# Kernel optimization log

Measured on AMD Instinct MI355X. Metric: run time of the kernel, lower is better.

The kernel has to match this reference:

```python
import math
import jax, jax.numpy as jnp
import numpy as np

D = 512
H = 8
N_COLS = 2048            # n + 1
D_COL = math.ceil(2 * math.log2(N_COLS))  # 22
B = 8
N_KEEP = 768
T = N_KEEP + 1


def setup_inputs() -> dict:
    key = jax.random.key(0)
    ks = jax.random.split(key, 12)
    inp = {
        "x_head": jax.random.normal(ks[0], (B, T, D), jnp.float32),
        "x_tail": jax.random.normal(ks[1], (B, T, D), jnp.float32),
        "ids_keep": jax.random.randint(ks[2], (B, N_KEEP), 0, N_COLS - 1),
        # W_tail is tied to W_head (sym_weight=True)
        "W_head_w": jax.random.normal(ks[3], (D, D), jnp.float32) * (1.0 / math.sqrt(D)),
        "W_head_b": jnp.zeros((D,), jnp.float32),
        "W_v_w": jax.random.normal(ks[4], (D, D), jnp.float32) * (1.0 / math.sqrt(D)),
        "W_v_b": jnp.zeros((D,), jnp.float32),
        "W_out_w": jax.random.normal(ks[5], (D, D), jnp.float32) * (1.0 / math.sqrt(D)),
        "W_out_b": jnp.zeros((D,), jnp.float32),
        "rel_emb": jnp.ones((H, D // H), jnp.float32),
        "col_head": jax.random.normal(ks[6], (H, N_COLS, D_COL), jnp.float32),
        "col_tail": jax.random.normal(ks[7], (H, N_COLS, D_COL), jnp.float32),
        "bias": jnp.zeros((1,), jnp.float32),
    }
    return inp


def _split_heads(x, n_heads):
    b, t, d = x.shape
    return x.reshape(b, t, n_heads, d // n_heads).transpose(0, 2, 1, 3)  # [B,H,T,dh]


def _gather_cols(col_emb, ids_keep):
    """col_emb: [H, N_COLS, d_col] (L2-normalized). Gather kept feature rows per
    batch element and re-prepend the CLS/readout row -> [B, H, 1+n_keep, d_col]."""
    cls = col_emb[:, :1, :]                       # [H,1,dc]
    feats = col_emb[:, 1:, :]                     # [H,N_COLS-1,dc]
    kept = jnp.take(feats, ids_keep, axis=1)      # [H,B,nk,dc]
    kept = kept.transpose(1, 0, 2, 3)             # [B,H,nk,dc]
    cls_b = jnp.broadcast_to(cls[None], (kept.shape[0],) + cls.shape)  # [B,H,1,dc]
    return jnp.concatenate([cls_b, kept], axis=2)


def reference(x_head, x_tail, ids_keep, W_head_w, W_head_b, W_v_w, W_v_b,
              W_out_w, W_out_b, rel_emb, col_head, col_tail, bias):
    n_heads = rel_emb.shape[0]
    d_head = rel_emb.shape[1]
    b, t, _ = x_head.shape

    # Projections (W_tail tied to W_head)
    f_head = x_head @ W_head_w.T + W_head_b
    f_tail = x_tail @ W_head_w.T + W_head_b
    f_v = x_tail @ W_v_w.T + W_v_b

    fh = _split_heads(f_head, n_heads)  # [B,H,T,dh]
    ft = _split_heads(f_tail, n_heads)
    fv = _split_heads(f_v, n_heads)

    # relation-weighted score: f_head @ diag(rel_emb) @ f_tail^T / sqrt(dh)
    weight_score = jnp.einsum('bhqd,bhkd->bhqk', fh * rel_emb[None, :, None, :], ft)
    weight_score = weight_score / math.sqrt(d_head)

    # Normalized topology embeddings + masked-token gather
    ch = col_head / jnp.linalg.norm(col_head, axis=-1, keepdims=True)
    ct = col_tail / jnp.linalg.norm(col_tail, axis=-1, keepdims=True)
    ch = _gather_cols(ch, ids_keep)  # [B,H,T,dc]
    ct = _gather_cols(ct, ids_keep)
    top_score = jnp.einsum('bhqd,bhkd->bhqk', ch, ct)  # [B,H,T,T]

    # Topology -> straight-through binary adjacency
    adj_probs = jax.nn.sigmoid(top_score + bias[0])
    nsi_mask = 1.0 - jnp.eye(t, dtype=adj_probs.dtype)          # no self-interaction
    adj_probs = adj_probs * nsi_mask
    readout_mask = jnp.ones((t,), adj_probs.dtype).at[0].set(0.0)  # prune edges to readout
    adj_probs = adj_probs * readout_mask
    adj = (adj_probs > 0.5).astype(adj_probs.dtype) - jax.lax.stop_gradient(adj_probs) + adj_probs

    adj_mask = (1.0 - adj) * -10000.0
    fr_graph = jax.nn.softmax(weight_score + adj_mask, axis=-1)

    x = jnp.einsum('bhqk,bhkd->bhqd', fr_graph, fv)
    x = x.transpose(0, 2, 1, 3).reshape(b, t, n_heads * fv.shape[-1])
    x = x @ W_out_w.T + W_out_b
    return (x, jax.lax.stop_gradient(fr_graph))
```

## Files before the change

### kernel.cpp

```cpp
#include <hip/hip_runtime.h>

#define D_     512
#define H_     8
#define NCOLS_ 2048
#define DCOL_  22
#define B_     8
#define NKEEP_ 768
#define T_     769
#define BT_    (B_*T_)
#define BH_    (B_*H_)

typedef __attribute__((ext_vector_type(8))) short bf16x8;
typedef __attribute__((ext_vector_type(8))) _Float16 f16x8;
typedef __attribute__((ext_vector_type(4))) float f32x4;

__device__ __forceinline__ ushort f2bf(float f) {
    unsigned u = __float_as_uint(f);
    unsigned r = u + 0x7fffu + ((u >> 16) & 1u);
    return (ushort)(r >> 16);
}
__device__ __forceinline__ float bf2f(ushort u) {
    return __uint_as_float(((unsigned)u) << 16);
}

__device__ __attribute__((noinline)) float exact_dot22(
    const float* __restrict__ qp, const float* __restrict__ kp)
{
    float s = 0.f;
    #pragma unroll
    for (int d2 = 0; d2 < DCOL_; ++d2) s += qp[d2]*kp[d2];
    return s;
}

__global__ __launch_bounds__(256) void pre_all(
    const float* __restrict__ xh, const float* __restrict__ xt,
    const float* __restrict__ Wh, const float* __restrict__ Wv,
    const float* __restrict__ bh_, const float* __restrict__ bv_,
    const float* __restrict__ rel,
    ushort* __restrict__ fhb, ushort* __restrict__ ftb,
    ushort* __restrict__ fvb,
    const float* __restrict__ col_head, const float* __restrict__ col_tail,
    const int* __restrict__ ids,
    float* __restrict__ chg, float* __restrict__ ctg,
    ushort* __restrict__ chH, ushort* __restrict__ chL,
    ushort* __restrict__ ctH, ushort* __restrict__ ctL)
{
    __shared__ __align__(16) ushort As[128*40];
    __shared__ __align__(16) ushort Bs[128*40];
    const int job = blockIdx.z;
    const int t   = threadIdx.x;

    if (job == 3) {
        const int total = BH_ * T_;
        const int stride = 4*49*256;
        for (int r = ((int)blockIdx.y*4 + (int)blockIdx.x)*256 + t;
             r < 2*total; r += stride) {
            const bool tail = (r >= total);
            int rr = tail ? r - total : r;
            int bh = rr / T_;
            int q  = rr - bh*T_;
            int b  = bh >> 3, h = bh & 7;
            int src = (q == 0) ? 0 : (1 + ids[b*NKEEP_ + q - 1]);
            const float* cp = (tail ? col_tail : col_head) + ((size_t)h*NCOLS_ + src)*DCOL_;
            float v[DCOL_];
            float ss = 0.f;
            #pragma unroll
            for (int j = 0; j < DCOL_; ++j) { v[j] = cp[j]; ss += v[j]*v[j]; }
            float inv = 1.0f / sqrtf(ss);
            float* op = (tail ? ctg : chg) + (size_t)rr*DCOL_;
            ushort* hp = (tail ? ctH : chH) + (size_t)rr*32;
            ushort* lp = (tail ? ctL : chL) + (size_t)rr*32;
            #pragma unroll
            for (int j = 0; j < DCOL_; ++j) {
                float x = v[j]*inv;
                op[j] = x;
                float xs = x * 32.f;
                _Float16 hh = (_Float16)xs;
                float res = (xs - (float)hh) * 2048.f;
                _Float16 ll = (_Float16)res;
                hp[j] = __builtin_bit_cast(ushort, hh);
                lp[j] = __builtin_bit_cast(ushort, ll);
            }
            #pragma unroll
            for (int j = DCOL_; j < 32; ++j) { hp[j] = 0; lp[j] = 0; }
        }
        return;
    }

    const float* A32; const float* W; const float* bias;
    ushort* outb; int mode;
    if (job == 0)      { A32 = xh; W = Wh; bias = bh_; outb = fhb; mode = 0; }
    else if (job == 1) { A32 = xt; W = Wh; bias = bh_; outb = ftb; mode = 1; }
    else               { A32 = xt; W = Wv; bias = bv_; outb = fvb; mode = 2; }

    const int lane = t & 63;
    const int wv   = t >> 6;
    const int wr   = wv >> 1, wc = wv & 1;
    const int m16  = lane & 15, q4 = lane >> 4;
    const int m0   = blockIdx.y * 128;
    const int n0   = blockIdx.x * 128;

    f32x4 acc[4][4] = {};
    for (int k0 = 0; k0 < 512; k0 += 32) {
        {
            const int sr = t >> 1, sh = t & 1;
            const int row = m0 + sr;
            ushort ta[16];
            #pragma unroll
            for (int e = 0; e < 16; ++e) ta[e] = 0;
            if (row < BT_) {
                const float* ap = A32 + (size_t)row*512 + k0 + sh*16;
                #pragma unroll
                for (int e = 0; e < 4; ++e) {
                    float4 f = *(const float4*)(ap + e*4);
                    ta[e*4+0]=f2bf(f.x); ta[e*4+1]=f2bf(f.y);
                    ta[e*4+2]=f2bf(f.z); ta[e*4+3]=f2bf(f.w);
                }
            }
            *(bf16x8*)&As[sr*40 + sh*16]     = *(bf16x8*)&ta[0];
            *(bf16x8*)&As[sr*40 + sh*16 + 8] = *(bf16x8*)&ta[8];
            const float* wp = W + (size_t)(n0 + sr)*512 + k0 + sh*16;
            ushort tw[16];
            #pragma unroll
            for (int e = 0; e < 4; ++e) {
                float4 f = *(const float4*)(wp + e*4);
                tw[e*4+0]=f2bf(f.x); tw[e*4+1]=f2bf(f.y);
                tw[e*4+2]=f2bf(f.z); tw[e*4+3]=f2bf(f.w);
            }
            *(bf16x8*)&Bs[sr*40 + sh*16]     = *(bf16x8*)&tw[0];
            *(bf16x8*)&Bs[sr*40 + sh*16 + 8] = *(bf16x8*)&tw[8];
        }
        __syncthreads();
        bf16x8 a[4], b[4];
        #pragma unroll
        for (int i = 0; i < 4; ++i)
            a[i] = *(const bf16x8*)&As[(wr*64 + i*16 + m16)*40 + q4*8];
        #pragma unroll
        for (int j = 0; j < 4; ++j)
            b[j] = *(const bf16x8*)&Bs[(wc*64 + j*16 + m16)*40 + q4*8];
        #pragma unroll
        for (int i = 0; i < 4; ++i)
            #pragma unroll
            for (int j = 0; j < 4; ++j)
                acc[i][j] = __builtin_amdgcn_mfma_f32_16x16x32_bf16(a[i], b[j], acc[i][j], 0, 0, 0);
        __syncthreads();
    }

    #pragma unroll
    for (int j = 0; j < 4; ++j) {
        const int n = n0 + wc*64 + j*16 + m16;
        const float bn = bias[n];
        const float sc = (mode == 0) ? rel[n] * 0.125f : 1.0f;
        const int h = n >> 6, dh = n & 63;
        #pragma unroll
        for (int i = 0; i < 4; ++i) {
            #pragma unroll
            for (int r = 0; r < 4; ++r) {
                int m = m0 + wr*64 + i*16 + q4*4 + r;
                if (m >= BT_) continue;
                float v = acc[i][j][r] + bn;
                if (mode == 0) v *= sc;
                int bb = m / T_, tt = m - bb*T_;
                outb[(((size_t)bb*H_ + h)*T_ + tt)*64 + dh] = f2bf(v);
            }
        }
    }
}

__global__ __launch_bounds__(256, 3) void fused_attn(
    const ushort* __restrict__ fhb, const ushort* __restrict__ ftb,
    const ushort* __restrict__ fvb, const float* __restrict__ chg,
    const float* __restrict__ ctg,
    const ushort* __restrict__ chH, const ushort* __restrict__ chL,
    const ushort* __restrict__ ctH, const ushort* __restrict__ ctL,
    const float* __restrict__ biasp,
    float* __restrict__ fr, ushort* __restrict__ x1b, float* __restrict__ invA)
{
    __shared__ __align__(16) ushort Qs[64*72];
    __shared__ __align__(16) ushort Ks[64*72];
    __shared__ __align__(16) ushort Vs[64*72];
    __shared__ __align__(16) ushort Et[64*72];
    __shared__ __align__(16) ushort KH[64*40];
    __shared__ __align__(16) ushort KL[64*40];
    __shared__ float sumP[4*64];
    __shared__ float inv_s[64];

    const int bh = blockIdx.y;
    const int q0 = blockIdx.x * 64;

    const int t    = threadIdx.x;
    const int lane = t & 63, w = t >> 6;
    const int m16  = lane & 15, q4 = lane >> 4;
    const float bias0 = biasp[0];

    {
        int qr = t >> 2, qc = min(q0 + qr, T_-1);
        const ushort* qp = fhb + ((size_t)bh*T_ + qc)*64 + (t&3)*16;
        *(bf16x8*)&Qs[qr*72 + (t&3)*16]     = *(const bf16x8*)qp;
        *(bf16x8*)&Qs[qr*72 + (t&3)*16 + 8] = *(const bf16x8*)(qp + 8);
    }
    f16x8 gqh[4], gql[4];
    #pragma unroll
    for (int i = 0; i < 4; ++i) {
        int qc = min(q0 + i*16 + m16, T_-1);
        gqh[i] = *(const f16x8*)(chH + ((size_t)bh*T_ + qc)*32 + q4*8);
        gql[i] = *(const f16x8*)(chL + ((size_t)bh*T_ + qc)*32 + q4*8);
    }

    float psum[4][4] = {};
    f32x4 Oacc[4] = {};

    for (int kt = 0; kt < 13; ++kt) {
        const int k0g = kt*64;
        __syncthreads();

        {
            int kr = t >> 2, kc = min(k0g + kr, T_-1);
            const ushort* kp = ftb + ((size_t)bh*T_ + kc)*64 + (t&3)*16;
            *(bf16x8*)&Ks[kr*72 + (t&3)*16]     = *(const bf16x8*)kp;
            *(bf16x8*)&Ks[kr*72 + (t&3)*16 + 8] = *(const bf16x8*)(kp + 8);
            const ushort* vp = fvb + ((size_t)bh*T_ + kc)*64 + (t&3)*16;
            bf16x8 v0 = *(const bf16x8*)vp, v1 = *(const bf16x8*)(vp + 8);
            const int dbase = (t&3)*16;
            #pragma unroll
            for (int e = 0; e < 8; ++e) {
                int d = dbase + e;
                Vs[d*72 + (((kr>>3) ^ (d>>3))<<3) + (kr&7)] = (ushort)v0[e];
            }
            #pragma unroll
            for (int e = 0; e < 8; ++e) {
                int d = dbase + 8 + e;
                Vs[d*72 + (((kr>>3) ^ (d>>3))<<3) + (kr&7)] = (ushort)v1[e];
            }
            const ushort* hp = ctH + ((size_t)bh*T_ + kc)*32 + (t&3)*8;
            const ushort* lp = ctL + ((size_t)bh*T_ + kc)*32 + (t&3)*8;
            *(bf16x8*)&KH[kr*40 + (t&3)*8] = *(const bf16x8*)hp;
            *(bf16x8*)&KL[kr*40 + (t&3)*8] = *(const bf16x8*)lp;
        }
        __syncthreads();

        const int kL2 = w*16 + m16;
        const int kg  = k0g + kL2;
        unsigned kmask = 0;
        {
            f16x8 bhf = *(const f16x8*)&KH[kL2*40 + q4*8];
            f16x8 blf = *(const f16x8*)&KL[kL2*40 + q4*8];
            f32x4 G1[4] = {}; f32x4 G2[4] = {};
            #pragma unroll
            for (int i = 0; i < 4; ++i) {
                G1[i] = __builtin_amdgcn_mfma_f32_16x16x32_f16(gqh[i], bhf, G1[i], 0, 0, 0);
                G2[i] = __builtin_amdgcn_mfma_f32_16x16x32_f16(gqh[i], blf, G2[i], 0, 0, 0);
                G2[i] = __builtin_amdgcn_mfma_f32_16x16x32_f16(gql[i], bhf, G2[i], 0, 0, 0);
            }
            const bool kok = (kg != 0) && (kg < T_);
            if (kok) {
                const float bS = bias0 * 1024.f;
                #pragma unroll
                for (int i = 0; i < 4; ++i) {
                    #pragma unroll
                    for (int r = 0; r < 4; ++r) {
                        int qg = q0 + i*16 + q4*4 + r;
                        if (qg == kg) continue;
                        float sd = G1[i][r] + G2[i][r]*(1.0f/2048.0f) + bS;
                        bool keep = sd > 0.f;
                        if (__builtin_fabsf(sd) <= 0.16f && qg < T_) {
                            float s = exact_dot22(chg + ((size_t)bh*T_ + qg)*DCOL_,
                                                  ctg + ((size_t)bh*T_ + kg)*DCOL_);
                            keep = (s + bias0 > 0.f);
                        }
                        if (keep) kmask |= 1u << (i*4 + r);
                    }
                }
            }
        }

        f32x4 Sacc[4] = {};
        #pragma unroll
        for (int step = 0; step < 2; ++step) {
            bf16x8 b = *(const bf16x8*)&Ks[kL2*72 + step*32 + q4*8];
            #pragma unroll
            for (int i = 0; i < 4; ++i) {
                bf16x8 a = *(const bf16x8*)&Qs[(i*16 + m16)*72 + step*32 + q4*8];
                Sacc[i] = __builtin_amdgcn_mfma_f32_16x16x32_bf16(a, b, Sacc[i], 0, 0, 0);
            }
        }

        #pragma unroll
        for (int i = 0; i < 4; ++i) {
            #pragma unroll
            for (int r = 0; r < 4; ++r) {
                float e = ((kmask >> (i*4 + r)) & 1u) ? __expf(Sacc[i][r]) : 0.f;
                psum[i][r] += e;
                Et[(i*16 + q4*4 + r)*72 + kL2] = f2bf(e);
            }
        }
        __syncthreads();

        #pragma unroll
        for (int step = 0; step < 2; ++step) {
            bf16x8 a = *(const bf16x8*)&Et[(w*16 + m16)*72 + step*32 + q4*8];
            #pragma unroll
            for (int j = 0; j < 4; ++j) {
                int dv = j*16 + m16;
                bf16x8 b = *(const bf16x8*)&Vs[dv*72 + (((step*4 + q4) ^ (dv>>3))<<3)];
                Oacc[j] = __builtin_amdgcn_mfma_f32_16x16x32_bf16(a, b, Oacc[j], 0, 0, 0);
            }
        }

        {
            const int c = t & 15;
            #pragma unroll
            for (int p = 0; p < 4; ++p) {
                int row = p*16 + (t >> 4);
                int qg = q0 + row;
                if (qg >= T_) continue;
                char* rowbase = (char*)(fr + ((size_t)bh*T_ + qg)*T_);
                #pragma unroll
                for (int e = 0; e < 2; ++e) {
                    int dw = c + 16*e;
                    int kk = k0g + dw*2;
                    unsigned u = *(const unsigned*)&Et[row*72 + dw*2];
                    if (kk + 1 < T_)
                        __builtin_nontemporal_store(u, (unsigned*)(rowbase + (size_t)kk*2));
                    else if (kk < T_)
                        __builtin_nontemporal_store((ushort)u, (ushort*)(rowbase + (size_t)kk*2));
                }
            }
        }
    }

    #pragma unroll
    for (int i = 0; i < 4; ++i)
        #pragma unroll
        for (int r = 0; r < 4; ++r) {
            float v = psum[i][r];
            v += __shfl_xor(v, 1, 64);
            v += __shfl_xor(v, 2, 64);
            v += __shfl_xor(v, 4, 64);
            v += __shfl_xor(v, 8, 64);
            psum[i][r] = v;
        }
    if (m16 == 0) {
        #pragma unroll
        for (int i = 0; i < 4; ++i)
            #pragma unroll
            for (int r = 0; r < 4; ++r)
                sumP[w*64 + i*16 + q4*4 + r] = psum[i][r];
    }
    __syncthreads();
    if (t < 64) {
        float s = sumP[t] + sumP[64+t] + sumP[128+t] + sumP[192+t];
        float iv = 1.0f / fmaxf(s, 1e-30f);
        inv_s[t] = iv;
        if (q0 + t < T_) invA[(size_t)bh*T_ + q0 + t] = iv;
    }
    __syncthreads();

    {
        const int b = bh >> 3, h = bh & 7;
        #pragma unroll
        for (int j = 0; j < 4; ++j) {
            int d = j*16 + m16;
            #pragma unroll
            for (int r = 0; r < 4; ++r) {
                int rr = w*16 + q4*4 + r;
                int qg = q0 + rr;
                if (qg < T_)
                    x1b[((size_t)b*T_ + qg)*512 + h*64 + d] = f2bf(Oacc[j][r] * inv_s[rr]);
            }
        }
    }
}

__global__ __launch_bounds__(256) void post_all(
    const ushort* __restrict__ x1b, const float* __restrict__ Wo,
    const float* __restrict__ bo_,
    float* __restrict__ xout, float* __restrict__ fr,
    const float* __restrict__ invA)
{
    __shared__ __align__(16) ushort As[128*40];
    __shared__ __align__(16) ushort Bs[128*40];
    const int bid = blockIdx.x;
    const int t   = threadIdx.x;

    if (bid >= 196) {
        const int row = bid - 196;
        float* rowp = fr + (size_t)row * T_;
        const ushort* packed = (const ushort*)rowp;
        const float iv = invA[row];
        float v0 = bf2f(packed[t])       * iv;
        float v1 = bf2f(packed[t + 256]) * iv;
        float v2 = bf2f(packed[t + 512]) * iv;
        float v3 = 0.f;
        if (t == 0) v3 = bf2f(packed[768]) * iv;
        __syncthreads();
        __builtin_nontemporal_store(v0, rowp + t);
        __builtin_nontemporal_store(v1, rowp + t + 256);
        __builtin_nontemporal_store(v2, rowp + t + 512);
        if (t == 0) __builtin_nontemporal_store(v3, rowp + 768);
        return;
    }

    const int lane = t & 63;
    const int wv   = t >> 6;
    const int wr   = wv >> 1, wc = wv & 1;
    const int m16  = lane & 15, q4 = lane >> 4;
    const int n0   = (bid & 3) * 128;
    const int m0   = (bid >> 2) * 128;

    f32x4 acc[4][4] = {};
    for (int k0 = 0; k0 < 512; k0 += 32) {
        {
            const int sr = t >> 1, sh = t & 1;
            const int row = m0 + sr;
            bf16x8 z = {}; bf16x8 v0 = z, v1 = z;
            if (row < BT_) {
                const bf16x8* gp = (const bf16x8*)(x1b + (size_t)row*512 + k0 + sh*16);
                v0 = gp[0]; v1 = gp[1];
            }
            *(bf16x8*)&As[sr*40 + sh*16]     = v0;
            *(bf16x8*)&As[sr*40 + sh*16 + 8] = v1;
            const float* wp = Wo + (size_t)(n0 + sr)*512 + k0 + sh*16;
            ushort tw[16];
            #pragma unroll
            for (int e = 0; e < 4; ++e) {
                float4 f = *(const float4*)(wp + e*4);
                tw[e*4+0]=f2bf(f.x); tw[e*4+1]=f2bf(f.y);
                tw[e*4+2]=f2bf(f.z); tw[e*4+3]=f2bf(f.w);
            }
            *(bf16x8*)&Bs[sr*40 + sh*16]     = *(bf16x8*)&tw[0];
            *(bf16x8*)&Bs[sr*40 + sh*16 + 8] = *(bf16x8*)&tw[8];
        }
        __syncthreads();
        bf16x8 a[4], b[4];
        #pragma unroll
        for (int i = 0; i < 4; ++i)
            a[i] = *(const bf16x8*)&As[(wr*64 + i*16 + m16)*40 + q4*8];
        #pragma unroll
        for (int j = 0; j < 4; ++j)
            b[j] = *(const bf16x8*)&Bs[(wc*64 + j*16 + m16)*40 + q4*8];
        #pragma unroll
        for (int i = 0; i < 4; ++i)
            #pragma unroll
            for (int j = 0; j < 4; ++j)
                acc[i][j] = __builtin_amdgcn_mfma_f32_16x16x32_bf16(a[i], b[j], acc[i][j], 0, 0, 0);
        __syncthreads();
    }

    #pragma unroll
    for (int j = 0; j < 4; ++j) {
        const int n = n0 + wc*64 + j*16 + m16;
        const float bn = bo_[n];
        #pragma unroll
        for (int i = 0; i < 4; ++i) {
            #pragma unroll
            for (int r = 0; r < 4; ++r) {
                int m = m0 + wr*64 + i*16 + q4*4 + r;
                if (m >= BT_) continue;
                __builtin_nontemporal_store(acc[i][j][r] + bn, xout + (size_t)m*512 + n);
            }
        }
    }
}

extern "C" void kernel_launch(void* const* d_in, const int* in_sizes, int n_in,
                              void* d_out, int out_size, void* d_ws, size_t ws_size,
                              hipStream_t stream)
{
    (void)in_sizes; (void)n_in; (void)out_size; (void)ws_size;
    const float* x_head   = (const float*)d_in[0];
    const float* x_tail   = (const float*)d_in[1];
    const int*   ids      = (const int*)  d_in[2];
    const float* W_head_w = (const float*)d_in[3];
    const float* W_head_b = (const float*)d_in[4];
    const float* W_v_w    = (const float*)d_in[5];
    const float* W_v_b    = (const float*)d_in[6];
    const float* W_out_w  = (const float*)d_in[7];
    const float* W_out_b  = (const float*)d_in[8];
    const float* rel      = (const float*)d_in[9];
    const float* col_h    = (const float*)d_in[10];
    const float* col_t    = (const float*)d_in[11];
    const float* biasp    = (const float*)d_in[12];

    const size_t F   = (size_t)BH_*T_*64;
    const size_t C22 = (size_t)BH_*T_*DCOL_;
    const size_t C32 = (size_t)BH_*T_*32;

    char* ws = (char*)d_ws;
    ushort* fhb = (ushort*)ws;   ws += F*2;
    ushort* ftb = (ushort*)ws;   ws += F*2;
    ushort* fvb = (ushort*)ws;   ws += F*2;
    ushort* x1b = (ushort*)ws;   ws += F*2;
    float*  chg = (float*)ws;    ws += C22*4;
    float*  ctg = (float*)ws;    ws += C22*4;
    float*  invA = (float*)ws;   ws += (size_t)BH_*T_*4;
    ushort* chH = (ushort*)ws;   ws += C32*2;
    ushort* chL = (ushort*)ws;   ws += C32*2;
    ushort* ctH = (ushort*)ws;   ws += C32*2;
    ushort* ctL = (ushort*)ws;   ws += C32*2;

    float* xout = (float*)d_out;
    float* fr   = xout + (size_t)BT_*D_;

    dim3 blk(256, 1, 1);

    pre_all<<<dim3(4, 49, 4), blk, 0, stream>>>(
        x_head, x_tail, W_head_w, W_v_w, W_head_b, W_v_b, rel,
        fhb, ftb, fvb,
        col_h, col_t, ids, chg, ctg, chH, chL, ctH, ctL);

    fused_attn<<<dim3(13, BH_), blk, 0, stream>>>(
        fhb, ftb, fvb, chg, ctg, chH, chL, ctH, ctL, biasp, fr, x1b, invA);

    post_all<<<dim3(196 + BH_*T_, 1, 1), blk, 0, stream>>>(
        x1b, W_out_w, W_out_b, xout, fr, invA);
}
```

Measured before the change: 529.2 us.

## Compute fp16 hi/lo splits of column embeddings on the fly inside attention

Removes the precomputed fp16 hi/lo split buffers (chH/chL/ctH/ctL). pre_all now writes only the normalized fp32 embeddings, and fused_attn reads those and does the hi/lo split in registers when it loads query fragments and stages key tiles into LDS, zeroing the padding columns once. It also switches the fr output stores from nontemporal to ordinary stores. This trades extra global traffic for per-tile conversion ALU work repeated across the 13 query blocks, and the change of store type may alter cache behaviour for the large fr output.

```diff
diff --git a/kernel.cpp b/kernel.cpp
--- a/kernel.cpp
+++ b/kernel.cpp
@@ -32,6 +32,14 @@
     return s;
 }
 
+__device__ __forceinline__ void hilo(float x, ushort& h, ushort& l) {
+    float xs = x * 32.f;
+    _Float16 hh = (_Float16)xs;
+    _Float16 ll = (_Float16)((xs - (float)hh) * 2048.f);
+    h = __builtin_bit_cast(ushort, hh);
+    l = __builtin_bit_cast(ushort, ll);
+}
+
 __global__ __launch_bounds__(256) void pre_all(
     const float* __restrict__ xh, const float* __restrict__ xt,
     const float* __restrict__ Wh, const float* __restrict__ Wv,
@@ -41,9 +49,7 @@
     ushort* __restrict__ fvb,
     const float* __restrict__ col_head, const float* __restrict__ col_tail,
     const int* __restrict__ ids,
-    float* __restrict__ chg, float* __restrict__ ctg,
-    ushort* __restrict__ chH, ushort* __restrict__ chL,
-    ushort* __restrict__ ctH, ushort* __restrict__ ctL)
+    float* __restrict__ chg, float* __restrict__ ctg)
 {
     __shared__ __align__(16) ushort As[128*40];
     __shared__ __align__(16) ushort Bs[128*40];
@@ -68,21 +74,8 @@
             for (int j = 0; j < DCOL_; ++j) { v[j] = cp[j]; ss += v[j]*v[j]; }
             float inv = 1.0f / sqrtf(ss);
             float* op = (tail ? ctg : chg) + (size_t)rr*DCOL_;
-            ushort* hp = (tail ? ctH : chH) + (size_t)rr*32;
-            ushort* lp = (tail ? ctL : chL) + (size_t)rr*32;
-            #pragma unroll
-            for (int j = 0; j < DCOL_; ++j) {
-                float x = v[j]*inv;
-                op[j] = x;
-                float xs = x * 32.f;
-                _Float16 hh = (_Float16)xs;
-                float res = (xs - (float)hh) * 2048.f;
-                _Float16 ll = (_Float16)res;
-                hp[j] = __builtin_bit_cast(ushort, hh);
-                lp[j] = __builtin_bit_cast(ushort, ll);
-            }
-            #pragma unroll
-            for (int j = DCOL_; j < 32; ++j) { hp[j] = 0; lp[j] = 0; }
+            #pragma unroll
+            for (int j = 0; j < DCOL_; ++j) op[j] = v[j]*inv;
         }
         return;
     }
@@ -170,10 +163,7 @@
 __global__ __launch_bounds__(256, 3) void fused_attn(
     const ushort* __restrict__ fhb, const ushort* __restrict__ ftb,
     const ushort* __restrict__ fvb, const float* __restrict__ chg,
-    const float* __restrict__ ctg,
-    const ushort* __restrict__ chH, const ushort* __restrict__ chL,
-    const ushort* __restrict__ ctH, const ushort* __restrict__ ctL,
-    const float* __restrict__ biasp,
+    const float* __restrict__ ctg, const float* __restrict__ biasp,
     float* __restrict__ fr, ushort* __restrict__ x1b, float* __restrict__ invA)
 {
     __shared__ __align__(16) ushort Qs[64*72];
@@ -193,6 +183,12 @@
     const int m16  = lane & 15, q4 = lane >> 4;
     const float bias0 = biasp[0];
 
+    for (int idx = t; idx < 64*5; idx += 256) {
+        int r5 = idx / 5, c = idx - r5*5;
+        *(unsigned*)&KH[r5*40 + 22 + c*2] = 0u;
+        *(unsigned*)&KL[r5*40 + 22 + c*2] = 0u;
+    }
+
     {
         int qr = t >> 2, qc = min(q0 + qr, T_-1);
         const ushort* qp = fhb + ((size_t)bh*T_ + qc)*64 + (t&3)*16;
@@ -202,9 +198,24 @@
     f16x8 gqh[4], gql[4];
     #pragma unroll
     for (int i = 0; i < 4; ++i) {
+        f16x8 zh = {}; f16x8 zl = {};
         int qc = min(q0 + i*16 + m16, T_-1);
-        gqh[i] = *(const f16x8*)(chH + ((size_t)bh*T_ + qc)*32 + q4*8);
-        gql[i] = *(const f16x8*)(chL + ((size_t)bh*T_ + qc)*32 + q4*8);
+        const float* cq = chg + ((size_t)bh*T_ + qc)*DCOL_;
+        const int base = q4*8;
+        #pragma unroll
+        for (int e = 0; e < 8; e += 2) {
+            int d = base + e;
+            if (d + 1 < DCOL_) {
+                float2 xy = *(const float2*)(cq + d);
+                ushort h0,l0,h1,l1;
+                hilo(xy.x, h0, l0); hilo(xy.y, h1, l1);
+                zh[e]   = __builtin_bit_cast(_Float16, h0);
+                zh[e+1] = __builtin_bit_cast(_Float16, h1);
+                zl[e]   = __builtin_bit_cast(_Float16, l0);
+                zl[e+1] = __builtin_bit_cast(_Float16, l1);
+            }
+        }
+        gqh[i] = zh; gql[i] = zl;
     }
 
     float psum[4][4] = {};
@@ -216,12 +227,13 @@
 
         {
             int kr = t >> 2, kc = min(k0g + kr, T_-1);
-            const ushort* kp = ftb + ((size_t)bh*T_ + kc)*64 + (t&3)*16;
-            *(bf16x8*)&Ks[kr*72 + (t&3)*16]     = *(const bf16x8*)kp;
-            *(bf16x8*)&Ks[kr*72 + (t&3)*16 + 8] = *(const bf16x8*)(kp + 8);
-            const ushort* vp = fvb + ((size_t)bh*T_ + kc)*64 + (t&3)*16;
+            const int sh = t & 3;
+            const ushort* kp = ftb + ((size_t)bh*T_ + kc)*64 + sh*16;
+            *(bf16x8*)&Ks[kr*72 + sh*16]     = *(const bf16x8*)kp;
+            *(bf16x8*)&Ks[kr*72 + sh*16 + 8] = *(const bf16x8*)(kp + 8);
+            const ushort* vp = fvb + ((size_t)bh*T_ + kc)*64 + sh*16;
             bf16x8 v0 = *(const bf16x8*)vp, v1 = *(const bf16x8*)(vp + 8);
-            const int dbase = (t&3)*16;
+            const int dbase = sh*16;
             #pragma unroll
             for (int e = 0; e < 8; ++e) {
                 int d = dbase + e;
@@ -232,10 +244,16 @@
                 int d = dbase + 8 + e;
                 Vs[d*72 + (((kr>>3) ^ (d>>3))<<3) + (kr&7)] = (ushort)v1[e];
             }
-            const ushort* hp = ctH + ((size_t)bh*T_ + kc)*32 + (t&3)*8;
-            const ushort* lp = ctL + ((size_t)bh*T_ + kc)*32 + (t&3)*8;
-            *(bf16x8*)&KH[kr*40 + (t&3)*8] = *(const bf16x8*)hp;
-            *(bf16x8*)&KL[kr*40 + (t&3)*8] = *(const bf16x8*)lp;
+            const float* cg = ctg + ((size_t)bh*T_ + kc)*DCOL_;
+            const int ds = sh*6;
+            const int dn = (sh < 3) ? 6 : 4;
+            for (int jj = 0; jj < dn; jj += 2) {
+                float2 xy = *(const float2*)(cg + ds + jj);
+                ushort h0,l0,h1,l1;
+                hilo(xy.x, h0, l0); hilo(xy.y, h1, l1);
+                *(unsigned*)&KH[kr*40 + ds + jj] = (unsigned)h0 | ((unsigned)h1 << 16);
+                *(unsigned*)&KL[kr*40 + ds + jj] = (unsigned)l0 | ((unsigned)l1 << 16);
+            }
         }
         __syncthreads();
 
@@ -320,10 +338,8 @@
                     int dw = c + 16*e;
                     int kk = k0g + dw*2;
                     unsigned u = *(const unsigned*)&Et[row*72 + dw*2];
-                    if (kk + 1 < T_)
-                        __builtin_nontemporal_store(u, (unsigned*)(rowbase + (size_t)kk*2));
-                    else if (kk < T_)
-                        __builtin_nontemporal_store((ushort)u, (ushort*)(rowbase + (size_t)kk*2));
+                    if (kk + 1 < T_)      *(unsigned*)(rowbase + (size_t)kk*2) = u;
+                    else if (kk < T_)     *(ushort*)(rowbase + (size_t)kk*2) = (ushort)u;
                 }
             }
         }
@@ -484,7 +500,6 @@
 
     const size_t F   = (size_t)BH_*T_*64;
     const size_t C22 = (size_t)BH_*T_*DCOL_;
-    const size_t C32 = (size_t)BH_*T_*32;
 
     char* ws = (char*)d_ws;
     ushort* fhb = (ushort*)ws;   ws += F*2;
@@ -494,10 +509,6 @@
     float*  chg = (float*)ws;    ws += C22*4;
     float*  ctg = (float*)ws;    ws += C22*4;
     float*  invA = (float*)ws;   ws += (size_t)BH_*T_*4;
-    ushort* chH = (ushort*)ws;   ws += C32*2;
-    ushort* chL = (ushort*)ws;   ws += C32*2;
-    ushort* ctH = (ushort*)ws;   ws += C32*2;
-    ushort* ctL = (ushort*)ws;   ws += C32*2;
 
     float* xout = (float*)d_out;
     float* fr   = xout + (size_t)BT_*D_;
@@ -507,10 +518,10 @@
     pre_all<<<dim3(4, 49, 4), blk, 0, stream>>>(
         x_head, x_tail, W_head_w, W_v_w, W_head_b, W_v_b, rel,
         fhb, ftb, fvb,
-        col_h, col_t, ids, chg, ctg, chH, chL, ctH, ctL);
+        col_h, col_t, ids, chg, ctg);
 
     fused_attn<<<dim3(13, BH_), blk, 0, stream>>>(
-        fhb, ftb, fvb, chg, ctg, chH, chL, ctH, ctL, biasp, fr, x1b, invA);
+        fhb, ftb, fvb, chg, ctg, biasp, fr, x1b, invA);
 
     post_all<<<dim3(196 + BH_*T_, 1, 1), blk, 0, stream>>>(
         x1b, W_out_w, W_out_b, xout, fr, invA);
```

Measured after the change: 660.5 us. 1.25x slower.
